# Performance work log

Hardware: AMD Instinct MI355X
Metric: run time of the kernel (lower is better)

## Reference

```python
import jax, jax.numpy as jnp
import numpy as np

DECAY = 0.99
EPS = 1e-05


def setup_inputs() -> dict:
    key = jax.random.key(0)
    k1, k2, k3 = jax.random.split(key, 3)
    x = jax.random.normal(k1, (16, 4096, 512), dtype=jnp.float32)
    embed = jax.random.normal(k2, (1024, 512), dtype=jnp.float32)
    cluster_size = jnp.ones((1024,), dtype=jnp.float32)
    embed_avg = jax.random.normal(k3, (1024, 512), dtype=jnp.float32)
    return {"x": x, "embed": embed, "cluster_size": cluster_size, "embed_avg": embed_avg}


def reference(x, embed, cluster_size, embed_avg):
    # x: [..., d]; embed: [K, d]
    K, d = embed.shape
    xf = x.reshape(-1, d)  # [N, d]
    dist = -(jnp.sum(xf * xf, axis=1, keepdims=True)
             - 2.0 * (xf @ embed.T)
             + jnp.sum(embed * embed, axis=1)[None, :])  # [N, K]
    ind = jnp.argmax(dist, axis=-1)  # [N]
    quantize = embed[ind].reshape(x.shape)  # dequantize (embedding lookup)
    embed_ind = ind.reshape(x.shape[:-1])
    # Training-mode EMA updates (one-hot scatter expressed as segment adds)
    counts = jnp.zeros((K,), dtype=x.dtype).at[ind].add(1.0)           # onehot.sum(0)
    embed_sum = jnp.zeros((K, d), dtype=x.dtype).at[ind].add(xf)       # (x^T @ onehot)^T
    new_cluster_size = cluster_size * DECAY + (1.0 - DECAY) * counts
    new_embed_avg = embed_avg * DECAY + (1.0 - DECAY) * embed_sum
    n = jnp.sum(new_cluster_size)
    cs = (new_cluster_size + EPS) / (n + K * EPS) * n  # laplace smoothing * total
    new_embed = new_embed_avg / cs[:, None]
    return (quantize, embed_ind, new_cluster_size, new_embed_avg, new_embed)
```

## Files before the change

### kernel.cpp

```cpp
#include <hip/hip_runtime.h>

typedef unsigned short ushort_t;
typedef __attribute__((ext_vector_type(8))) short bf16x8;
typedef __attribute__((ext_vector_type(4))) float f32x4;

#define DECAY 0.99f
#define EPS 1e-5f
#define K_CODES 1024
#define D 512
#define N_ROWS 65536
#define MARGIN 0.4f

#define BM 128
#define NKT 8
#define NCH 16

#define FG 8

#define CHUNK 64
#define MAX_CHUNKS 2048

#define XH_OFF   0u
#define EH_OFF   134217728u
#define ESUM_OFF 136314880u
#define CNT_OFF  138412032u
#define E2_OFF   138416128u
#define NFLAG_OFF 138420224u
#define NPTR_OFF  138420228u
#define FLAGS_OFF 138420480u
#define WS_NEED  (138420480u + 262144u)
#define ROWLIST_OFF   0u
#define BASE_OFF      262144u
#define CURSOR_OFF    266240u
#define CHUNKBASE_OFF 270336u
#define DESC_OFF      274432u
#define PARTIAL_OFF   307200u

__device__ inline ushort_t f2bf(float f) {
    unsigned int u = __float_as_uint(f);
    unsigned int r = (u + 0x7FFFu + ((u >> 16) & 1u)) >> 16;
    return (ushort_t)r;
}

__device__ inline void gload16_lds(const void* g, void* l) {
    __builtin_amdgcn_global_load_lds(
        (const __attribute__((address_space(1))) unsigned int*)g,
        (__attribute__((address_space(3))) unsigned int*)l, 16, 0, 0);
}

__global__ __launch_bounds__(256) void prep_hi(const float* __restrict__ src,
                                               ushort_t* __restrict__ hi) {
    const int g = blockIdx.x * 256 + threadIdx.x;
    const int ln = g & 63;
    const int tc = g >> 6;
    const int C = tc & 15;
    const int R = tc >> 4;
    const int row = (R << 4) + (ln & 15);
    const int k = (C << 5) + ((ln >> 4) << 3);
    const float4 v0 = *(const float4*)(src + (size_t)row * D + k);
    const float4 v1 = *(const float4*)(src + (size_t)row * D + k + 4);
    float v[8] = {v0.x, v0.y, v0.z, v0.w, v1.x, v1.y, v1.z, v1.w};
    short h[8];
    #pragma unroll
    for (int i = 0; i < 8; ++i) h[i] = (short)f2bf(v[i]);
    bf16x8 hv = {h[0], h[1], h[2], h[3], h[4], h[5], h[6], h[7]};
    *(bf16x8*)(hi + (size_t)g * 8) = hv;
}

__global__ __launch_bounds__(64) void e2_kernel(const float* __restrict__ embed,
                                                float* __restrict__ e2) {
    const int k = blockIdx.x;
    const int t = threadIdx.x;
    const float* row = embed + (size_t)k * D;
    float s = 0.f;
    #pragma unroll
    for (int i = 0; i < D / 64; ++i) {
        float v = row[t + 64 * i];
        s = fmaf(v, v, s);
    }
    #pragma unroll
    for (int off = 32; off; off >>= 1) s += __shfl_down(s, off, 64);
    if (t == 0) e2[k] = s;
}

__global__ __launch_bounds__(256, 1) void vq_main(const ushort_t* __restrict__ xh,
                                                  const ushort_t* __restrict__ eh,
                                                  const float* __restrict__ embed,
                                                  const float* __restrict__ e2,
                                                  float* __restrict__ out_q,
                                                  float* __restrict__ out_ind,
                                                  float* __restrict__ counts,
                                                  int* __restrict__ nflag,
                                                  int* __restrict__ flags) {
    __shared__ short sA[65536];
    __shared__ short sB[2][4096];
    __shared__ float se2[1024];
    __shared__ float red_b[128][2], red_s[128][2];
    __shared__ int   red_i[128][2];
    __shared__ int   bestk[128];

    const int tid = threadIdx.x;
    const int lane = tid & 63;
    const int w = tid >> 6;
    const int wm = w & 1;
    const int wn = w >> 1;
    const int bid = (int)blockIdx.x;
    const int R0 = bid * 8;
    const int row0 = bid * BM;

    for (int i = tid; i < 1024; i += 256) se2[i] = e2[i];

    const int ltile = lane << 3;

    #pragma unroll
    for (int i = 0; i < 32; ++i) {
        const int tt = (w << 5) + i;
        const int c = tt >> 3;
        const int t = tt & 7;
        gload16_lds(xh + ((size_t)((R0 + t) * 16 + c) << 9) + ltile, sA + (tt << 9));
    }
    {
        #pragma unroll
        for (int t2 = 0; t2 < 2; ++t2) {
            const int t = (w << 1) + t2;
            gload16_lds(eh + ((size_t)(t * 16 + 0) << 9) + ltile, sB[0] + (t << 9));
        }
    }
    __syncthreads();
    int cur = 0;

    float tb[16], ts[16];
    int ti[16];
    #pragma unroll
    for (int s = 0; s < 16; ++s) { tb[s] = -3.4e38f; ts[s] = -3.4e38f; ti[s] = 0; }

    for (int kt = 0; kt < NKT; ++kt) {
        f32x4 acc[4][4];
        #pragma unroll
        for (int mt = 0; mt < 4; ++mt)
            #pragma unroll
            for (int nt = 0; nt < 4; ++nt) acc[mt][nt] = (f32x4){0.f, 0.f, 0.f, 0.f};

        for (int c = 0; c < NCH; ++c) {
            const int nxt = cur ^ 1;
            if (!(kt == NKT - 1 && c == NCH - 1)) {
                const int nk = (c == NCH - 1) ? kt + 1 : kt;
                const int nc = (c == NCH - 1) ? 0 : c + 1;
                #pragma unroll
                for (int t2 = 0; t2 < 2; ++t2) {
                    const int t = (w << 1) + t2;
                    gload16_lds(eh + ((size_t)(((nk << 3) + t) * 16 + nc) << 9) + ltile,
                                sB[nxt] + (t << 9));
                }
            }

            bf16x8 ah[4], bh[4];
            #pragma unroll
            for (int i = 0; i < 4; ++i) {
                ah[i] = *(const bf16x8*)(sA + (((c << 3) + (wm << 2) + i) << 9) + ltile);
                bh[i] = *(const bf16x8*)(sB[cur] + (((wn << 2) + i) << 9) + ltile);
            }
            #pragma unroll
            for (int nt = 0; nt < 4; ++nt) {
                #pragma unroll
                for (int mt = 0; mt < 4; ++mt) {
                    acc[mt][nt] = __builtin_amdgcn_mfma_f32_16x16x32_bf16(ah[mt], bh[nt], acc[mt][nt], 0, 0, 0);
                }
            }
            __syncthreads();
            cur = nxt;
        }

        #pragma unroll
        for (int nt = 0; nt < 4; ++nt) {
            const int code = (kt << 7) + (wn << 6) + (nt << 4) + (lane & 15);
            const float h = se2[code];
            #pragma unroll
            for (int mt = 0; mt < 4; ++mt) {
                #pragma unroll
                for (int r = 0; r < 4; ++r) {
                    const float v = fmaf(-0.5f, h, acc[mt][nt][r]);
                    const int s = (mt << 2) + r;
                    if (v > tb[s]) { ts[s] = tb[s]; tb[s] = v; ti[s] = code; }
                    else if (v > ts[s]) ts[s] = v;
                }
            }
        }
    }

    #pragma unroll
    for (int m = 1; m <= 8; m <<= 1) {
        #pragma unroll
        for (int s = 0; s < 16; ++s) {
            const float ob = __shfl_xor(tb[s], m, 64);
            const float os = __shfl_xor(ts[s], m, 64);
            const int oi = __shfl_xor(ti[s], m, 64);
            if (ob > tb[s] || (ob == tb[s] && oi < ti[s])) {
                ts[s] = fmaxf(tb[s], os); tb[s] = ob; ti[s] = oi;
            } else {
                ts[s] = fmaxf(ts[s], ob);
            }
        }
    }
    if ((lane & 15) == 0) {
        const int q = lane >> 4;
        #pragma unroll
        for (int mt = 0; mt < 4; ++mt)
            #pragma unroll
            for (int r = 0; r < 4; ++r) {
                const int rl = wm * 64 + mt * 16 + q * 4 + r;
                const int s = (mt << 2) + r;
                red_b[rl][wn] = tb[s]; red_s[rl][wn] = ts[s]; red_i[rl][wn] = ti[s];
            }
    }
    __syncthreads();

    if (tid < BM) {
        float b0 = red_b[tid][0], b1 = red_b[tid][1];
        float s0 = red_s[tid][0], s1 = red_s[tid][1];
        int i0 = red_i[tid][0], i1 = red_i[tid][1];
        float b, sec; int bi;
        if (b0 > b1 || (b0 == b1 && i0 < i1)) { b = b0; bi = i0; sec = fmaxf(s0, b1); }
        else { b = b1; bi = i1; sec = fmaxf(s1, b0); }
        bestk[tid] = bi;
        out_ind[row0 + tid] = (float)bi;
        atomicAdd(counts + bi, 1.0f);
        if (b - sec < MARGIN) {
            const int p = atomicAdd(nflag, 1);
            flags[p] = row0 + tid;
        }
    }
    __syncthreads();

    {
        const int f4 = tid & 127;
        const int rodd = tid >> 7;
        for (int it = 0; it < 64; ++it) {
            const int r = 2 * it + rodd;
            const int bk = bestk[r];
            const float4 q = ((const float4*)(embed + (size_t)bk * D))[f4];
            ((float4*)(out_q + (size_t)(row0 + r) * D))[f4] = q;
        }
    }
}

__global__ __launch_bounds__(256) void fixup(const float* __restrict__ x,
                                             const float* __restrict__ embed,
                                             const float* __restrict__ e2,
                                             const int* __restrict__ nflag,
                                             const int* __restrict__ flags,
                                             float* __restrict__ out_ind,
                                             float* __restrict__ out_q,
                                             float* __restrict__ counts) {
    __shared__ float xs[FG][512];
    __shared__ float wred_s[4][FG];
    __shared__ int   wred_i[4][FG];
    __shared__ int   s_new[FG];
    const int tid = threadIdx.x;
    const int lane = tid & 63;
    const int w = tid >> 6;
    const int n = *nflag;
    for (int g = blockIdx.x; g * FG < n; g += gridDim.x) {
        const int base = g * FG;
        const int cnt = min(FG, n - base);
        for (int i = tid; i < FG * 128; i += 256) {
            const int r = i >> 7, f4 = i & 127;
            float4 v = make_float4(0.f, 0.f, 0.f, 0.f);
            if (r < cnt) v = ((const float4*)(x + (size_t)flags[base + r] * D))[f4];
            ((float4*)xs[r])[f4] = v;
        }
        __syncthreads();

        float acc[4][FG];
        #pragma unroll
        for (int j = 0; j < 4; ++j)
            #pragma unroll
            for (int r = 0; r < FG; ++r) acc[j][r] = 0.f;
        for (int i4 = 0; i4 < 128; ++i4) {
            float4 xv[FG];
            #pragma unroll
            for (int r = 0; r < FG; ++r) xv[r] = ((const float4*)xs[r])[i4];
            #pragma unroll
            for (int j = 0; j < 4; ++j) {
                const float4 ev = ((const float4*)(embed + (size_t)(tid * 4 + j) * D))[i4];
                #pragma unroll
                for (int r = 0; r < FG; ++r) {
                    acc[j][r] = fmaf(ev.x, xv[r].x, acc[j][r]);
                    acc[j][r] = fmaf(ev.y, xv[r].y, acc[j][r]);
                    acc[j][r] = fmaf(ev.z, xv[r].z, acc[j][r]);
                    acc[j][r] = fmaf(ev.w, xv[r].w, acc[j][r]);
                }
            }
        }
        float bs[FG]; int bi[FG];
        #pragma unroll
        for (int r = 0; r < FG; ++r) { bs[r] = -3.4e38f; bi[r] = 0x7FFFFFFF; }
        #pragma unroll
        for (int j = 0; j < 4; ++j) {
            const int c = tid * 4 + j;
            const float he = -0.5f * e2[c];
            #pragma unroll
            for (int r = 0; r < FG; ++r) {
                const float v = acc[j][r] + he;
                if (v > bs[r] || (v == bs[r] && c < bi[r])) { bs[r] = v; bi[r] = c; }
            }
        }
        #pragma unroll
        for (int off = 1; off < 64; off <<= 1) {
            #pragma unroll
            for (int r = 0; r < FG; ++r) {
                const float os = __shfl_xor(bs[r], off, 64);
                const int oi = __shfl_xor(bi[r], off, 64);
                if (os > bs[r] || (os == bs[r] && oi < bi[r])) { bs[r] = os; bi[r] = oi; }
            }
        }
        if (lane == 0) {
            #pragma unroll
            for (int r = 0; r < FG; ++r) { wred_s[w][r] = bs[r]; wred_i[w][r] = bi[r]; }
        }
        __syncthreads();
        if (tid < FG) {
            float b = wred_s[0][tid]; int bidx = wred_i[0][tid];
            #pragma unroll
            for (int w2 = 1; w2 < 4; ++w2) {
                const float os = wred_s[w2][tid]; const int oi = wred_i[w2][tid];
                if (os > b || (os == b && oi < bidx)) { b = os; bidx = oi; }
            }
            int sn = -1;
            if (tid < cnt) {
                const int row = flags[base + tid];
                const int oldi = (int)out_ind[row];
                if (bidx != oldi) {
                    out_ind[row] = (float)bidx;
                    atomicAdd(counts + oldi, -1.0f);
                    atomicAdd(counts + bidx, 1.0f);
                    sn = bidx;
                }
            }
            s_new[tid] = sn;
        }
        __syncthreads();
        #pragma unroll
        for (int r = 0; r < FG; ++r) {
            const int nw = s_new[r];
            if (nw >= 0 && tid < 128) {
                ((float4*)(out_q + (size_t)flags[base + r] * D))[tid] =
                    ((const float4*)(embed + (size_t)nw * D))[tid];
            }
        }
        __syncthreads();
    }
}

__global__ __launch_bounds__(1024) void scan_kernel(const float* __restrict__ counts,
                                                    int* __restrict__ base,
                                                    int* __restrict__ cursor,
                                                    int* __restrict__ chunk_base,
                                                    int4* __restrict__ desc) {
    __shared__ int s[1024];
    const int t = threadIdx.x;
    const int c = (int)counts[t];
    s[t] = c;
    __syncthreads();
    #pragma unroll
    for (int off = 1; off < 1024; off <<= 1) {
        const int v = (t >= off) ? s[t - off] : 0;
        __syncthreads();
        s[t] += v;
        __syncthreads();
    }
    const int b = s[t] - c;
    base[t] = b;
    cursor[t] = b;
    const int nch = (c + CHUNK - 1) / CHUNK;
    s[t] = nch;
    __syncthreads();
    #pragma unroll
    for (int off = 1; off < 1024; off <<= 1) {
        const int v = (t >= off) ? s[t - off] : 0;
        __syncthreads();
        s[t] += v;
        __syncthreads();
    }
    const int cb = s[t] - nch;
    chunk_base[t] = cb;
    if (t == 1023) chunk_base[1024] = s[t];
    for (int j = 0; j < nch; ++j) {
        const int start = b + j * CHUNK;
        const int len = min(CHUNK, c - j * CHUNK);
        desc[cb + j] = make_int4(t, start, len, 0);
    }
}

__global__ __launch_bounds__(256) void scatter_kernel(const float* __restrict__ out_ind,
                                                      int* __restrict__ cursor,
                                                      int* __restrict__ rowlist) {
    const int g = blockIdx.x * 256 + threadIdx.x;
    const int code = (int)out_ind[g];
    const int pos = atomicAdd(cursor + code, 1);
    rowlist[pos] = g;
}

__global__ __launch_bounds__(128) void esum_partial(const float* __restrict__ x,
                                                    const int* __restrict__ chunk_base,
                                                    const int4* __restrict__ desc,
                                                    const int* __restrict__ rowlist,
                                                    float* __restrict__ partial) {
    const int b = blockIdx.x;
    if (b >= chunk_base[1024]) return;
    const int t = threadIdx.x;
    const int4 d = desc[b];
    const int b0 = d.y;
    const int cnt = d.z;
    float4 a0 = {0.f, 0.f, 0.f, 0.f}, a1 = {0.f, 0.f, 0.f, 0.f};
    float4 a2 = {0.f, 0.f, 0.f, 0.f}, a3 = {0.f, 0.f, 0.f, 0.f};
    int i = 0;
    for (; i + 4 <= cnt; i += 4) {
        const int r0 = rowlist[b0 + i];
        const int r1 = rowlist[b0 + i + 1];
        const int r2 = rowlist[b0 + i + 2];
        const int r3 = rowlist[b0 + i + 3];
        const float4 v0 = ((const float4*)x)[(size_t)r0 * 128 + t];
        const float4 v1 = ((const float4*)x)[(size_t)r1 * 128 + t];
        const float4 v2 = ((const float4*)x)[(size_t)r2 * 128 + t];
        const float4 v3 = ((const float4*)x)[(size_t)r3 * 128 + t];
        a0.x += v0.x; a0.y += v0.y; a0.z += v0.z; a0.w += v0.w;
        a1.x += v1.x; a1.y += v1.y; a1.z += v1.z; a1.w += v1.w;
        a2.x += v2.x; a2.y += v2.y; a2.z += v2.z; a2.w += v2.w;
        a3.x += v3.x; a3.y += v3.y; a3.z += v3.z; a3.w += v3.w;
    }
    for (; i < cnt; ++i) {
        const int r = rowlist[b0 + i];
        const float4 v = ((const float4*)x)[(size_t)r * 128 + t];
        a0.x += v.x; a0.y += v.y; a0.z += v.z; a0.w += v.w;
    }
    float4 s;
    s.x = (a0.x + a1.x) + (a2.x + a3.x);
    s.y = (a0.y + a1.y) + (a2.y + a3.y);
    s.z = (a0.z + a1.z) + (a2.z + a3.z);
    s.w = (a0.w + a1.w) + (a2.w + a3.w);
    ((float4*)partial)[(size_t)b * 128 + t] = s;
}

__global__ __launch_bounds__(128) void esum_final(const int* __restrict__ chunk_base,
                                                  const float* __restrict__ partial,
                                                  float* __restrict__ embed_sum) {
    const int k = blockIdx.x;
    const int t = threadIdx.x;
    const int c0 = chunk_base[k];
    const int c1 = chunk_base[k + 1];
    float4 a = {0.f, 0.f, 0.f, 0.f};
    for (int c = c0; c < c1; ++c) {
        const float4 v = ((const float4*)partial)[(size_t)c * 128 + t];
        a.x += v.x; a.y += v.y; a.z += v.z; a.w += v.w;
    }
    ((float4*)embed_sum)[(size_t)k * 128 + t] = a;
}

__global__ __launch_bounds__(256) void ema_cs(const float* __restrict__ cs,
                                              const float* __restrict__ counts,
                                              float* __restrict__ out_cs,
                                              float* __restrict__ nout) {
    __shared__ float red[256];
    const int t = threadIdx.x;
    const float4 c4 = ((const float4*)counts)[t];
    const float4 s4 = ((const float4*)cs)[t];
    float4 nc;
    nc.x = s4.x * DECAY + (1.f - DECAY) * c4.x;
    nc.y = s4.y * DECAY + (1.f - DECAY) * c4.y;
    nc.z = s4.z * DECAY + (1.f - DECAY) * c4.z;
    nc.w = s4.w * DECAY + (1.f - DECAY) * c4.w;
    ((float4*)out_cs)[t] = nc;
    red[t] = nc.x + nc.y + nc.z + nc.w;
    __syncthreads();
    #pragma unroll
    for (int off = 128; off; off >>= 1) {
        if (t < off) red[t] += red[t + off];
        __syncthreads();
    }
    if (t == 0) nout[0] = red[0];
}

__global__ __launch_bounds__(256) void ema_embed(const float* __restrict__ eavg,
                                                 const float* __restrict__ esum,
                                                 const float* __restrict__ ncs,
                                                 const float* __restrict__ nptr,
                                                 float* __restrict__ out_avg,
                                                 float* __restrict__ out_embed) {
    const int i4 = blockIdx.x * 256 + threadIdx.x;
    const int k = i4 >> 7;
    const float n = *nptr;
    const float csk = (ncs[k] + EPS) / (n + (float)K_CODES * EPS) * n;
    const float inv = 1.f / csk;
    const float4 a = ((const float4*)eavg)[i4];
    const float4 s = ((const float4*)esum)[i4];
    float4 na;
    na.x = a.x * DECAY + (1.f - DECAY) * s.x;
    na.y = a.y * DECAY + (1.f - DECAY) * s.y;
    na.z = a.z * DECAY + (1.f - DECAY) * s.z;
    na.w = a.w * DECAY + (1.f - DECAY) * s.w;
    ((float4*)out_avg)[i4] = na;
    float4 ne;
    ne.x = na.x * inv; ne.y = na.y * inv; ne.z = na.z * inv; ne.w = na.w * inv;
    ((float4*)out_embed)[i4] = ne;
}

#define MT2 128
#define S_STRIDE 132
__global__ __launch_bounds__(256, 2) void vq_main_f32(const float* __restrict__ x,
                                                      const float* __restrict__ embed,
                                                      const float* __restrict__ e2,
                                                      float* __restrict__ out_q,
                                                      float* __restrict__ out_ind,
                                                      float* __restrict__ counts,
                                                      float* __restrict__ embed_sum) {
    __shared__ float xs[32][S_STRIDE];
    __shared__ float es[32][S_STRIDE];
    __shared__ float rsc[MT2][17];
    __shared__ int rid[MT2][17];
    __shared__ int bestk[MT2];
    const int tid = threadIdx.x;
    const int lane = tid & 63;
    const int w = tid >> 6;
    const int tyg = (w & 1) * 8 + (lane >> 3);
    const int txg = (w >> 1) * 8 + (lane & 7);
    const int r0 = 8 * tyg, c0 = 8 * txg;
    const int row0 = blockIdx.x * MT2;
    const int sr = tid >> 3, sq = tid & 7;
    float best_s[8]; int best_i[8];
    #pragma unroll
    for (int r = 0; r < 8; ++r) { best_s[r] = -3.4e38f; best_i[r] = 0; }
    float4 px[4], pe[4];
    #pragma unroll
    for (int i = 0; i < 4; ++i) {
        px[i] = *(const float4*)(x + (size_t)(row0 + sr + 32 * i) * D + sq * 4);
        pe[i] = *(const float4*)(embed + (size_t)(sr + 32 * i) * D + sq * 4);
    }
    for (int kt = 0; kt < 8; ++kt) {
        const int k0 = kt * 128;
        float acc[8][8];
        #pragma unroll
        for (int j = 0; j < 8; ++j) {
            const float he = -0.5f * e2[k0 + c0 + j];
            #pragma unroll
            for (int r = 0; r < 8; ++r) acc[r][j] = he;
        }
        for (int dt = 0; dt < 16; ++dt) {
            __syncthreads();
            #pragma unroll
            for (int i = 0; i < 4; ++i) {
                const int rr = sr + 32 * i;
                #pragma unroll
                for (int ii = 0; ii < 4; ++ii) {
                    xs[sq * 4 + ii][rr] = ((const float*)&px[i])[ii];
                    es[sq * 4 + ii][rr] = ((const float*)&pe[i])[ii];
                }
            }
            __syncthreads();
            {
                const int s2 = kt * 16 + dt + 1;
                int kt2 = s2 >> 4; if (kt2 > 7) kt2 = 7;
                const int dt2 = s2 & 15;
                const int dof = dt2 * 32 + sq * 4;
                #pragma unroll
                for (int i = 0; i < 4; ++i) {
                    px[i] = *(const float4*)(x + (size_t)(row0 + sr + 32 * i) * D + dof);
                    pe[i] = *(const float4*)(embed + (size_t)(kt2 * 128 + sr + 32 * i) * D + dof);
                }
            }
            #pragma unroll 4
            for (int d = 0; d < 32; ++d) {
                const float4 xa = *(const float4*)&xs[d][r0];
                const float4 xb = *(const float4*)&xs[d][r0 + 4];
                const float4 ea = *(const float4*)&es[d][c0];
                const float4 eb = *(const float4*)&es[d][c0 + 4];
                const float xv[8] = {xa.x, xa.y, xa.z, xa.w, xb.x, xb.y, xb.z, xb.w};
                const float evv[8] = {ea.x, ea.y, ea.z, ea.w, eb.x, eb.y, eb.z, eb.w};
                #pragma unroll
                for (int r = 0; r < 8; ++r)
                    #pragma unroll
                    for (int j = 0; j < 8; ++j)
                        acc[r][j] = fmaf(xv[r], evv[j], acc[r][j]);
            }
        }
        #pragma unroll
        for (int j = 0; j < 8; ++j) {
            const int k = k0 + c0 + j;
            #pragma unroll
            for (int r = 0; r < 8; ++r)
                if (acc[r][j] > best_s[r]) { best_s[r] = acc[r][j]; best_i[r] = k; }
        }
    }
    #pragma unroll
    for (int r = 0; r < 8; ++r) { rsc[r0 + r][txg] = best_s[r]; rid[r0 + r][txg] = best_i[r]; }
    __syncthreads();
    if (tid < MT2) {
        float bs = rsc[tid][0]; int bk = rid[tid][0];
        #pragma unroll
        for (int g = 1; g < 16; ++g) {
            const float s = rsc[tid][g]; const int kk = rid[tid][g];
            if (s > bs || (s == bs && kk < bk)) { bs = s; bk = kk; }
        }
        bestk[tid] = bk;
        out_ind[row0 + tid] = (float)bk;
        atomicAdd(counts + bk, 1.0f);
    }
    __syncthreads();
    {
        const int f4 = tid & 127, rodd = tid >> 7;
        for (int it = 0; it < 64; ++it) {
            const int r = 2 * it + rodd;
            const int bk = bestk[r];
            const float4 q = ((const float4*)(embed + (size_t)bk * D))[f4];
            ((float4*)(out_q + (size_t)(row0 + r) * D))[f4] = q;
            const float4 xv = ((const float4*)(x + (size_t)(row0 + r) * D))[f4];
            float* sdst = embed_sum + (size_t)bk * D + f4 * 4;
            atomicAdd(sdst + 0, xv.x);
            atomicAdd(sdst + 1, xv.y);
            atomicAdd(sdst + 2, xv.z);
            atomicAdd(sdst + 3, xv.w);
        }
    }
}

extern "C" void kernel_launch(void* const* d_in, const int* in_sizes, int n_in,
                              void* d_out, int out_size, void* d_ws, size_t ws_size,
                              hipStream_t stream) {
    const float* x     = (const float*)d_in[0];
    const float* embed = (const float*)d_in[1];
    const float* cs    = (const float*)d_in[2];
    const float* eavg  = (const float*)d_in[3];

    float* out = (float*)d_out;
    float* out_q   = out;
    float* out_ind = out_q + (size_t)N_ROWS * D;
    float* out_cs  = out_ind + N_ROWS;
    float* out_avg = out_cs + K_CODES;
    float* out_emb = out_avg + (size_t)K_CODES * D;

    unsigned char* w = (unsigned char*)d_ws;

    if (ws_size >= WS_NEED) {
        ushort_t* xh = (ushort_t*)(w + XH_OFF);
        ushort_t* eh = (ushort_t*)(w + EH_OFF);
        float* esum  = (float*)(w + ESUM_OFF);
        float* counts = (float*)(w + CNT_OFF);
        float* e2    = (float*)(w + E2_OFF);
        int* nflag   = (int*)(w + NFLAG_OFF);
        float* nptr  = (float*)(w + NPTR_OFF);
        int* flags   = (int*)(w + FLAGS_OFF);
        int* rowlist    = (int*)(w + ROWLIST_OFF);
        int* base       = (int*)(w + BASE_OFF);
        int* cursor     = (int*)(w + CURSOR_OFF);
        int* chunk_base = (int*)(w + CHUNKBASE_OFF);
        int4* desc      = (int4*)(w + DESC_OFF);
        float* partial  = (float*)(w + PARTIAL_OFF);

        hipMemsetAsync(counts, 0, 4096, stream);
        hipMemsetAsync(nflag, 0, 4, stream);
        prep_hi<<<16384, 256, 0, stream>>>(x, xh);
        prep_hi<<<256, 256, 0, stream>>>(embed, eh);
        e2_kernel<<<K_CODES, 64, 0, stream>>>(embed, e2);
        vq_main<<<N_ROWS / BM, 256, 0, stream>>>(xh, eh, embed, e2,
                                                 out_q, out_ind, counts, nflag, flags);
        fixup<<<2048, 256, 0, stream>>>(x, embed, e2, nflag, flags,
                                        out_ind, out_q, counts);
        scan_kernel<<<1, 1024, 0, stream>>>(counts, base, cursor, chunk_base, desc);
        scatter_kernel<<<N_ROWS / 256, 256, 0, stream>>>(out_ind, cursor, rowlist);
        esum_partial<<<MAX_CHUNKS, 128, 0, stream>>>(x, chunk_base, desc, rowlist, partial);
        esum_final<<<K_CODES, 128, 0, stream>>>(chunk_base, partial, esum);
        ema_cs<<<1, 256, 0, stream>>>(cs, counts, out_cs, nptr);
        ema_embed<<<(K_CODES * D / 4) / 256, 256, 0, stream>>>(eavg, esum, out_cs, nptr,
                                                               out_avg, out_emb);
    } else {
        float* counts = (float*)w;
        float* esum = counts + K_CODES;
        float* e2 = esum + (size_t)K_CODES * D;
        float* nptr = e2 + K_CODES;
        hipMemsetAsync(counts, 0, (size_t)(K_CODES + K_CODES * D) * sizeof(float), stream);
        e2_kernel<<<K_CODES, 64, 0, stream>>>(embed, e2);
        vq_main_f32<<<N_ROWS / MT2, 256, 0, stream>>>(x, embed, e2, out_q, out_ind, counts, esum);
        ema_cs<<<1, 256, 0, stream>>>(cs, counts, out_cs, nptr);
        ema_embed<<<(K_CODES * D / 4) / 256, 256, 0, stream>>>(eavg, esum, out_cs, nptr,
                                                               out_avg, out_emb);
    }
}
```

Baseline: 841.2 us.

## Halve row tile, load codebook fragments directly to registers, run two blocks per CU

The row tile drops from 128 to 64 rows, and the shared-memory staging of codebook tiles is removed. Each wave now loads its B fragments straight from global memory into registers through a 4-stage software pipeline, which also removes the per-chunk __syncthreads. Each wave covers 32 codes across all 64 rows instead of a 2x2 wave split, and the cross-wave argmax reduction is widened to 4 partners. This raises occupancy (launch bounds 2) and cuts barrier overhead, at the cost of half the A-tile reuse per B fetch and more global/L2 traffic for the codebook.

```diff
diff --git a/kernel.cpp b/kernel.cpp
--- a/kernel.cpp
+++ b/kernel.cpp
@@ -11,7 +11,7 @@
 #define N_ROWS 65536
 #define MARGIN 0.4f
 
-#define BM 128
+#define BM 64
 #define NKT 8
 #define NCH 16
 
@@ -83,7 +83,7 @@
     if (t == 0) e2[k] = s;
 }
 
-__global__ __launch_bounds__(256, 1) void vq_main(const ushort_t* __restrict__ xh,
+__global__ __launch_bounds__(256, 2) void vq_main(const ushort_t* __restrict__ xh,
                                                   const ushort_t* __restrict__ eh,
                                                   const float* __restrict__ embed,
                                                   const float* __restrict__ e2,
@@ -92,20 +92,17 @@
                                                   float* __restrict__ counts,
                                                   int* __restrict__ nflag,
                                                   int* __restrict__ flags) {
-    __shared__ short sA[65536];
-    __shared__ short sB[2][4096];
+    __shared__ short sA[32768];
     __shared__ float se2[1024];
-    __shared__ float red_b[128][2], red_s[128][2];
-    __shared__ int   red_i[128][2];
-    __shared__ int   bestk[128];
+    __shared__ float red_b[64][4], red_s[64][4];
+    __shared__ int   red_i[64][4];
+    __shared__ int   bestk[64];
 
     const int tid = threadIdx.x;
     const int lane = tid & 63;
     const int w = tid >> 6;
-    const int wm = w & 1;
-    const int wn = w >> 1;
     const int bid = (int)blockIdx.x;
-    const int R0 = bid * 8;
+    const int R0 = bid * 4;
     const int row0 = bid * BM;
 
     for (int i = tid; i < 1024; i += 256) se2[i] = e2[i];
@@ -113,21 +110,37 @@
     const int ltile = lane << 3;
 
     #pragma unroll
-    for (int i = 0; i < 32; ++i) {
-        const int tt = (w << 5) + i;
-        const int c = tt >> 3;
-        const int t = tt & 7;
+    for (int i = 0; i < 16; ++i) {
+        const int tt = (w << 4) + i;
+        const int c = tt >> 2;
+        const int t = tt & 3;
         gload16_lds(xh + ((size_t)((R0 + t) * 16 + c) << 9) + ltile, sA + (tt << 9));
     }
-    {
-        #pragma unroll
-        for (int t2 = 0; t2 < 2; ++t2) {
-            const int t = (w << 1) + t2;
-            gload16_lds(eh + ((size_t)(t * 16 + 0) << 9) + ltile, sB[0] + (t << 9));
-        }
-    }
-    __syncthreads();
-    int cur = 0;
+
+    #define LOADB(P, nk, nc) do {                                                             \
+        P[0] = *(const bf16x8*)(eh + ((size_t)((((nk) << 3) + (w << 1) + 0) * 16 + (nc)) << 9) + ltile); \
+        P[1] = *(const bf16x8*)(eh + ((size_t)((((nk) << 3) + (w << 1) + 1) * 16 + (nc)) << 9) + ltile); \
+    } while (0)
+
+    #define COMPUTE(P, cc) do {                                                               \
+        bf16x8 ah0 = *(const bf16x8*)(sA + ((((cc) << 2) + 0) << 9) + ltile);                 \
+        bf16x8 ah1 = *(const bf16x8*)(sA + ((((cc) << 2) + 1) << 9) + ltile);                 \
+        bf16x8 ah2 = *(const bf16x8*)(sA + ((((cc) << 2) + 2) << 9) + ltile);                 \
+        bf16x8 ah3 = *(const bf16x8*)(sA + ((((cc) << 2) + 3) << 9) + ltile);                 \
+        acc[0][0] = __builtin_amdgcn_mfma_f32_16x16x32_bf16(ah0, P[0], acc[0][0], 0, 0, 0);   \
+        acc[1][0] = __builtin_amdgcn_mfma_f32_16x16x32_bf16(ah1, P[0], acc[1][0], 0, 0, 0);   \
+        acc[2][0] = __builtin_amdgcn_mfma_f32_16x16x32_bf16(ah2, P[0], acc[2][0], 0, 0, 0);   \
+        acc[3][0] = __builtin_amdgcn_mfma_f32_16x16x32_bf16(ah3, P[0], acc[3][0], 0, 0, 0);   \
+        acc[0][1] = __builtin_amdgcn_mfma_f32_16x16x32_bf16(ah0, P[1], acc[0][1], 0, 0, 0);   \
+        acc[1][1] = __builtin_amdgcn_mfma_f32_16x16x32_bf16(ah1, P[1], acc[1][1], 0, 0, 0);   \
+        acc[2][1] = __builtin_amdgcn_mfma_f32_16x16x32_bf16(ah2, P[1], acc[2][1], 0, 0, 0);   \
+        acc[3][1] = __builtin_amdgcn_mfma_f32_16x16x32_bf16(ah3, P[1], acc[3][1], 0, 0, 0);   \
+    } while (0)
+
+    bf16x8 p0[2], p1[2], p2[2], p3[2];
+    LOADB(p0, 0, 0);
+    LOADB(p1, 0, 1);
+    __syncthreads();
 
     float tb[16], ts[16];
     int ti[16];
@@ -135,45 +148,28 @@
     for (int s = 0; s < 16; ++s) { tb[s] = -3.4e38f; ts[s] = -3.4e38f; ti[s] = 0; }
 
     for (int kt = 0; kt < NKT; ++kt) {
-        f32x4 acc[4][4];
+        f32x4 acc[4][2];
         #pragma unroll
         for (int mt = 0; mt < 4; ++mt)
             #pragma unroll
-            for (int nt = 0; nt < 4; ++nt) acc[mt][nt] = (f32x4){0.f, 0.f, 0.f, 0.f};
-
-        for (int c = 0; c < NCH; ++c) {
-            const int nxt = cur ^ 1;
-            if (!(kt == NKT - 1 && c == NCH - 1)) {
-                const int nk = (c == NCH - 1) ? kt + 1 : kt;
-                const int nc = (c == NCH - 1) ? 0 : c + 1;
-                #pragma unroll
-                for (int t2 = 0; t2 < 2; ++t2) {
-                    const int t = (w << 1) + t2;
-                    gload16_lds(eh + ((size_t)(((nk << 3) + t) * 16 + nc) << 9) + ltile,
-                                sB[nxt] + (t << 9));
-                }
-            }
-
-            bf16x8 ah[4], bh[4];
-            #pragma unroll
-            for (int i = 0; i < 4; ++i) {
-                ah[i] = *(const bf16x8*)(sA + (((c << 3) + (wm << 2) + i) << 9) + ltile);
-                bh[i] = *(const bf16x8*)(sB[cur] + (((wn << 2) + i) << 9) + ltile);
-            }
-            #pragma unroll
-            for (int nt = 0; nt < 4; ++nt) {
-                #pragma unroll
-                for (int mt = 0; mt < 4; ++mt) {
-                    acc[mt][nt] = __builtin_amdgcn_mfma_f32_16x16x32_bf16(ah[mt], bh[nt], acc[mt][nt], 0, 0, 0);
-                }
-            }
-            __syncthreads();
-            cur = nxt;
-        }
-
-        #pragma unroll
-        for (int nt = 0; nt < 4; ++nt) {
-            const int code = (kt << 7) + (wn << 6) + (nt << 4) + (lane & 15);
+            for (int nt = 0; nt < 2; ++nt) acc[mt][nt] = (f32x4){0.f, 0.f, 0.f, 0.f};
+
+        for (int c = 0; c < NCH; c += 4) {
+            LOADB(p2, kt, c + 2);
+            COMPUTE(p0, c);
+            LOADB(p3, kt, c + 3);
+            COMPUTE(p1, c + 1);
+            if (c + 4 < NCH) { LOADB(p0, kt, c + 4); }
+            else if (kt + 1 < NKT) { LOADB(p0, kt + 1, 0); }
+            COMPUTE(p2, c + 2);
+            if (c + 4 < NCH) { LOADB(p1, kt, c + 5); }
+            else if (kt + 1 < NKT) { LOADB(p1, kt + 1, 1); }
+            COMPUTE(p3, c + 3);
+        }
+
+        #pragma unroll
+        for (int nt = 0; nt < 2; ++nt) {
+            const int code = (kt << 7) + (w << 5) + (nt << 4) + (lane & 15);
             const float h = se2[code];
             #pragma unroll
             for (int mt = 0; mt < 4; ++mt) {
@@ -187,6 +183,8 @@
             }
         }
     }
+    #undef LOADB
+    #undef COMPUTE
 
     #pragma unroll
     for (int m = 1; m <= 8; m <<= 1) {
@@ -208,20 +206,27 @@
         for (int mt = 0; mt < 4; ++mt)
             #pragma unroll
             for (int r = 0; r < 4; ++r) {
-                const int rl = wm * 64 + mt * 16 + q * 4 + r;
+                const int rl = mt * 16 + q * 4 + r;
                 const int s = (mt << 2) + r;
-                red_b[rl][wn] = tb[s]; red_s[rl][wn] = ts[s]; red_i[rl][wn] = ti[s];
+                red_b[rl][w] = tb[s]; red_s[rl][w] = ts[s]; red_i[rl][w] = ti[s];
             }
     }
     __syncthreads();
 
     if (tid < BM) {
-        float b0 = red_b[tid][0], b1 = red_b[tid][1];
-        float s0 = red_s[tid][0], s1 = red_s[tid][1];
-        int i0 = red_i[tid][0], i1 = red_i[tid][1];
-        float b, sec; int bi;
-        if (b0 > b1 || (b0 == b1 && i0 < i1)) { b = b0; bi = i0; sec = fmaxf(s0, b1); }
-        else { b = b1; bi = i1; sec = fmaxf(s1, b0); }
+        float b = red_b[tid][0], sec = red_s[tid][0];
+        int bi = red_i[tid][0];
+        #pragma unroll
+        for (int w2 = 1; w2 < 4; ++w2) {
+            const float ob = red_b[tid][w2];
+            const float os = red_s[tid][w2];
+            const int oi = red_i[tid][w2];
+            if (ob > b || (ob == b && oi < bi)) {
+                sec = fmaxf(b, os); b = ob; bi = oi;
+            } else {
+                sec = fmaxf(sec, ob);
+            }
+        }
         bestk[tid] = bi;
         out_ind[row0 + tid] = (float)bi;
         atomicAdd(counts + bi, 1.0f);
@@ -235,7 +240,7 @@
     {
         const int f4 = tid & 127;
         const int rodd = tid >> 7;
-        for (int it = 0; it < 64; ++it) {
+        for (int it = 0; it < 32; ++it) {
             const int r = 2 * it + rodd;
             const int bk = bestk[r];
             const float4 q = ((const float4*)(embed + (size_t)bk * D))[f4];
```

Result: no change. 843.3 us (+0.3%).
